# Kernel optimization log

Measured on AMD Instinct MI355X. Metric: run time of the kernel, lower is better.

Reference implementation:

```python
import jax, jax.numpy as jnp
import numpy as np


def setup_inputs() -> dict:
    key = jax.random.key(0)
    ks = jax.random.split(key, 4)
    B, S, D, U = 4, 4096, 128, 64
    x = jax.random.normal(ks[0], (B, S, D), dtype=jnp.float32)
    Wq = jax.random.normal(ks[1], (D, U), dtype=jnp.float32) * (1.0 / np.sqrt(D))
    Wk = jax.random.normal(ks[2], (D, U), dtype=jnp.float32) * (1.0 / np.sqrt(D))
    Wv = jax.random.normal(ks[3], (D, U), dtype=jnp.float32) * (1.0 / np.sqrt(D))
    bq = jnp.zeros((U,), dtype=jnp.float32)
    bk = jnp.zeros((U,), dtype=jnp.float32)
    bv = jnp.zeros((U,), dtype=jnp.float32)
    return {"x": x, "Wq": Wq, "bq": bq, "Wk": Wk, "bk": bk, "Wv": Wv, "bv": bv}


def reference(x, Wq, bq, Wk, bk, Wv, bv):
    # Single-head, unscaled, unmasked attention (faithful to the Keras layer).
    q = jnp.einsum("bsd,du->bsu", x, Wq) + bq  # [B,S,U]
    k = jnp.einsum("bsd,du->bsu", x, Wk) + bk  # [B,S,U]
    v = jnp.einsum("bsd,du->bsu", x, Wv) + bv  # [B,S,U]
    scores = jnp.einsum("bsu,btu->bst", q, k)  # [B,S,S], no 1/sqrt(d) scaling
    attn = jax.nn.softmax(scores, axis=-1)
    return jnp.einsum("bst,btu->bsu", attn, v)  # [B,S,U]
```

## Files before the change

### kernel.cpp

```cpp
#include <hip/hip_runtime.h>
#include <hip/hip_fp16.h>
#include <math.h>

#define SEQ   4096
#define DIM   128
#define UDIM  64
#define BATCH 4
#define BS    (BATCH*SEQ)

typedef _Float16 h8 __attribute__((ext_vector_type(8)));
typedef _Float16 h4 __attribute__((ext_vector_type(4)));
typedef _Float16 h2 __attribute__((ext_vector_type(2)));
typedef float    f4 __attribute__((ext_vector_type(4)));

#define MFMA_K32(a,b,c) __builtin_amdgcn_mfma_f32_16x16x32_f16((a),(b),(c),0,0,0)
#define MFMA_K16(a,b,c) __builtin_amdgcn_mfma_f32_16x16x16f16((a),(b),(c),0,0,0)

__device__ __forceinline__ h2 pk2(float a, float b) {
  return __builtin_bit_cast(h2, __builtin_amdgcn_cvt_pkrtz(a, b));
}
__device__ __forceinline__ float fexp2(float x) {
#if __has_builtin(__builtin_amdgcn_exp2f)
  return __builtin_amdgcn_exp2f(x);
#else
  return exp2f(x);
#endif
}

#define WT_STRIDE 272
#define KB_STRIDE 144
#define L2E 1.44269504088896f


__global__ __launch_bounds__(256, 3) void proj_mfma(
    const float* __restrict__ x,
    const float* __restrict__ Wq, const float* __restrict__ bq,
    const float* __restrict__ Wk, const float* __restrict__ bk,
    const float* __restrict__ Wv, const float* __restrict__ bv,
    _Float16* __restrict__ qf, _Float16* __restrict__ kswz, _Float16* __restrict__ vswz)
{
  const int proj = blockIdx.y;
  const float* __restrict__ W    = proj==0 ? Wq : (proj==1 ? Wk : Wv);
  const float* __restrict__ bias = proj==0 ? bq : (proj==1 ? bk : bv);
  const int tid  = threadIdx.x;
  const int lane = tid & 63, wv = tid >> 6;
  const int n = lane & 15, quad = lane >> 4;
  const int r0 = blockIdx.x * 64;

  __shared__ __align__(16) char lds[UDIM * WT_STRIDE];
  __shared__ __align__(16) char kbnc[4 * 16 * KB_STRIDE];

  #pragma unroll
  for (int i = 0; i < 8; ++i) {
    const int idx = i*256 + tid;
    const int nn  = idx & 63;
    const int k4  = (idx >> 6) * 4;
    const float w0 = W[(k4+0)*UDIM + nn];
    const float w1 = W[(k4+1)*UDIM + nn];
    const float w2 = W[(k4+2)*UDIM + nn];
    const float w3 = W[(k4+3)*UDIM + nn];
    int2 wd;
    wd.x = __builtin_bit_cast(int, pk2(w0, w1));
    wd.y = __builtin_bit_cast(int, pk2(w2, w3));
    *(int2*)(lds + nn*WT_STRIDE + k4*2) = wd;
  }
  __syncthreads();

  const int row = r0 + wv*16 + n;
  h8 xa[4];
  #pragma unroll
  for (int ks = 0; ks < 4; ++ks) {
    const float* xp = x + (size_t)row*DIM + ks*32 + quad*8;
    const f4 a = *(const f4*)xp, b = *(const f4*)(xp + 4);
    int4 pkd;
    pkd.x = __builtin_bit_cast(int, pk2(a[0], a[1]));
    pkd.y = __builtin_bit_cast(int, pk2(a[2], a[3]));
    pkd.z = __builtin_bit_cast(int, pk2(b[0], b[1]));
    pkd.w = __builtin_bit_cast(int, pk2(b[2], b[3]));
    xa[ks] = __builtin_bit_cast(h8, pkd);
  }

  f4 acc[4];
  #pragma unroll
  for (int nt = 0; nt < 4; ++nt) acc[nt] = (f4){0.f,0.f,0.f,0.f};

  #pragma unroll
  for (int ks = 0; ks < 4; ++ks)
    #pragma unroll
    for (int nt = 0; nt < 4; ++nt) {
      const h8 wf = *(const h8*)(lds + (nt*16 + n)*WT_STRIDE + (ks*32 + quad*8)*2);
      acc[nt] = MFMA_K32(xa[ks], wf, acc[nt]);
    }

  #pragma unroll
  for (int nt = 0; nt < 4; ++nt) {
    const float bb = bias[nt*16 + n];
    #pragma unroll
    for (int r = 0; r < 4; ++r) acc[nt][r] += bb;
  }

  const int b  = r0 / SEQ;
  const int kb = ((r0 % SEQ) >> 4) + wv;

  if (proj == 0) {
    #pragma unroll
    for (int nt = 0; nt < 4; ++nt)
      #pragma unroll
      for (int r = 0; r < 4; ++r) acc[nt][r] *= L2E;
    const int par = lane & 1;
    const unsigned sel = par ? 0x03020706u : 0x05040100u;
    #pragma unroll
    for (int nt = 0; nt < 4; ++nt)
      #pragma unroll
      for (int p = 0; p < 2; ++p) {
        const int r = 2*p;
        unsigned A  = __builtin_bit_cast(unsigned, pk2(acc[nt][r], acc[nt][r+1]));
        unsigned Bs = (unsigned)__builtin_amdgcn_mov_dpp((int)A, 0xB1, 0xF, 0xF, true);
        unsigned w  = __builtin_amdgcn_perm(Bs, A, sel);
        const int orow = r0 + wv*16 + 4*quad + r + par;
        const int ocol = nt*16 + n - par;
        *(unsigned*)((char*)qf + ((size_t)orow*UDIM + ocol)*2) = w;
      }
  } else if (proj == 1) {
    char* base = kbnc + wv*(16*KB_STRIDE);
    #pragma unroll
    for (int nt = 0; nt < 4; ++nt)
      #pragma unroll
      for (int r = 0; r < 4; ++r)
        *(_Float16*)(base + (4*quad + r)*KB_STRIDE + (nt*16 + n)*2) =
            (_Float16)acc[nt][r];
    _Float16* kdst = kswz + (size_t)b*SEQ*UDIM;
    #pragma unroll
    for (int ks = 0; ks < 2; ++ks) {
      const h8 f = *(const h8*)(base + n*KB_STRIDE + ks*64 + quad*16);
      *(h8*)(kdst + ((size_t)(kb*2 + ks)*64 + lane)*8) = f;
    }
  } else {
    _Float16* vdst = vswz + (size_t)b*SEQ*UDIM;
    #pragma unroll
    for (int pr = 0; pr < 2; ++pr) {
      int4 t;
      t.x = __builtin_bit_cast(int, pk2(acc[2*pr][0],   acc[2*pr][1]));
      t.y = __builtin_bit_cast(int, pk2(acc[2*pr][2],   acc[2*pr][3]));
      t.z = __builtin_bit_cast(int, pk2(acc[2*pr+1][0], acc[2*pr+1][1]));
      t.w = __builtin_bit_cast(int, pk2(acc[2*pr+1][2], acc[2*pr+1][3]));
      *(int4*)(vdst + ((size_t)(kb*2 + pr)*64 + lane)*8) = t;
    }
  }
}

__global__ __launch_bounds__(256, 4) void flash_attn_t(
    const _Float16* __restrict__ qf, const _Float16* __restrict__ kswz,
    const _Float16* __restrict__ vswz,
    _Float16* __restrict__ opart, float* __restrict__ Mp, float* __restrict__ Lp,
    int nkt)
{
  const int qt = blockIdx.x, b = blockIdx.y, sp = blockIdx.z;
  const int tid = threadIdx.x;
  const int lane = tid & 63, wid = tid >> 6;
  const int n = lane & 15, quad = lane >> 4;
  const int qbase = qt*128 + wid*32;

  const _Float16* __restrict__ qb = qf + (size_t)b*SEQ*UDIM;
  const _Float16* kpl = kswz + (size_t)b*SEQ*UDIM + (size_t)sp*nkt*4096 + lane*8;
  const _Float16* kph = kpl + 2048;
  const _Float16* vpl = vswz + (size_t)b*SEQ*UDIM + (size_t)sp*nkt*4096 + lane*8;
  const _Float16* vph = vpl + 2048;

  h8 qB[2][2];
  #pragma unroll
  for (int nt = 0; nt < 2; ++nt)
    #pragma unroll
    for (int ks = 0; ks < 2; ++ks)
      qB[nt][ks] = *(const h8*)(qb + (size_t)(qbase + nt*16 + n)*UDIM + ks*32 + quad*8);

  f4 O[4][2], Ol[2];
  #pragma unroll
  for (int ut = 0; ut < 4; ++ut)
    #pragma unroll
    for (int nt = 0; nt < 2; ++nt) O[ut][nt] = (f4){0.f,0.f,0.f,0.f};
  Ol[0] = (f4){0.f,0.f,0.f,0.f};
  Ol[1] = (f4){0.f,0.f,0.f,0.f};

  float M[2] = {-1e30f, -1e30f};

  h4 ones_a;
  { const _Float16 o = (_Float16)1.0f;
    ones_a[0]=o; ones_a[1]=o; ones_a[2]=o; ones_a[3]=o; }

  for (int t = 0; t < nkt; ++t) {
    h8 ka[4][2];
    ka[0][0] = *(const h8*)(kpl);        ka[0][1] = *(const h8*)(kpl +  512);
    ka[1][0] = *(const h8*)(kpl + 1024); ka[1][1] = *(const h8*)(kpl + 1536);
    ka[2][0] = *(const h8*)(kph);        ka[2][1] = *(const h8*)(kph +  512);
    ka[3][0] = *(const h8*)(kph + 1024); ka[3][1] = *(const h8*)(kph + 1536);

    h8 vc0 = *(const h8*)(vpl);
    h8 vc1 = *(const h8*)(vpl + 512);

    f4 S[4][2];
    #pragma unroll
    for (int mt = 0; mt < 4; ++mt)
      #pragma unroll
      for (int nt = 0; nt < 2; ++nt) S[mt][nt] = (f4){0.f,0.f,0.f,0.f};
    #pragma unroll
    for (int ks = 0; ks < 2; ++ks)
      #pragma unroll
      for (int mt = 0; mt < 4; ++mt)
        #pragma unroll
        for (int nt = 0; nt < 2; ++nt)
          S[mt][nt] = MFMA_K32(ka[mt][ks], qB[nt][ks], S[mt][nt]);

    float mn[2];
    #pragma unroll
    for (int nt = 0; nt < 2; ++nt) {
      float m0 = fmaxf(fmaxf(S[0][nt][0], S[0][nt][1]), fmaxf(S[0][nt][2], S[0][nt][3]));
      float m1 = fmaxf(fmaxf(S[1][nt][0], S[1][nt][1]), fmaxf(S[1][nt][2], S[1][nt][3]));
      float m2 = fmaxf(fmaxf(S[2][nt][0], S[2][nt][1]), fmaxf(S[2][nt][2], S[2][nt][3]));
      float m3 = fmaxf(fmaxf(S[3][nt][0], S[3][nt][1]), fmaxf(S[3][nt][2], S[3][nt][3]));
      float rm = fmaxf(fmaxf(m0, m1), fmaxf(m2, m3));
      rm = fmaxf(rm, __shfl_xor(rm, 16));
      rm = fmaxf(rm, __shfl_xor(rm, 32));
      mn[nt] = fmaxf(M[nt], rm);
    }

    const bool nochange = (mn[0] == M[0]) && (mn[1] == M[1]);
    if (!__all(nochange)) {
      #pragma unroll
      for (int nt = 0; nt < 2; ++nt) {
        const float alpha = fexp2(M[nt] - mn[nt]);
        #pragma unroll
        for (int ut = 0; ut < 4; ++ut)
          #pragma unroll
          for (int r = 0; r < 4; ++r) O[ut][nt][r] *= alpha;
        #pragma unroll
        for (int r = 0; r < 4; ++r) Ol[nt][r] *= alpha;
      }
    }
    M[0] = mn[0]; M[1] = mn[1];

    h4 pB[4][2];
    #pragma unroll
    for (int mt = 0; mt < 4; ++mt)
      #pragma unroll
      for (int nt = 0; nt < 2; ++nt) {
        #pragma unroll
        for (int r = 0; r < 4; ++r)
          S[mt][nt][r] = fexp2(S[mt][nt][r] - mn[nt]);
        int2 tt;
        tt.x = __builtin_bit_cast(int, pk2(S[mt][nt][0], S[mt][nt][1]));
        tt.y = __builtin_bit_cast(int, pk2(S[mt][nt][2], S[mt][nt][3]));
        pB[mt][nt] = __builtin_bit_cast(h4, tt);
      }

    #pragma unroll
    for (int mt = 0; mt < 4; ++mt) {
      h8 vn0, vn1;
      if (mt == 0) { vn0 = *(const h8*)(vpl + 1024); vn1 = *(const h8*)(vpl + 1536); }
      if (mt == 1) { vn0 = *(const h8*)(vph);        vn1 = *(const h8*)(vph +  512); }
      if (mt == 2) { vn0 = *(const h8*)(vph + 1024); vn1 = *(const h8*)(vph + 1536); }
      const int4 vi0 = __builtin_bit_cast(int4, vc0);
      const int4 vi1 = __builtin_bit_cast(int4, vc1);
      int2 p01, p23, p45, p67;
      p01.x = vi0.x; p01.y = vi0.y;  p23.x = vi0.z; p23.y = vi0.w;
      p45.x = vi1.x; p45.y = vi1.y;  p67.x = vi1.z; p67.y = vi1.w;
      h4 va[4];
      va[0] = __builtin_bit_cast(h4, p01);
      va[1] = __builtin_bit_cast(h4, p23);
      va[2] = __builtin_bit_cast(h4, p45);
      va[3] = __builtin_bit_cast(h4, p67);
      #pragma unroll
      for (int ut = 0; ut < 4; ++ut)
        #pragma unroll
        for (int nt = 0; nt < 2; ++nt)
          O[ut][nt] = MFMA_K16(va[ut], pB[mt][nt], O[ut][nt]);
      #pragma unroll
      for (int nt = 0; nt < 2; ++nt)
        Ol[nt] = MFMA_K16(ones_a, pB[mt][nt], Ol[nt]);
      if (mt < 3) { vc0 = vn0; vc1 = vn1; }
    }

    kpl += 4096; kph += 4096; vpl += 4096; vph += 4096;
  }

  const size_t rowg = (size_t)sp*BS + (size_t)b*SEQ + qbase;
  #pragma unroll
  for (int nt = 0; nt < 2; ++nt) {
    char* __restrict__ orow = (char*)(opart + (rowg + nt*16 + n)*UDIM);
    #pragma unroll
    for (int ut = 0; ut < 4; ++ut)
      #pragma unroll
      for (int p = 0; p < 2; ++p)
        *(unsigned*)(orow + (ut*16 + quad*4 + 2*p)*2) =
            __builtin_bit_cast(unsigned, pk2(O[ut][nt][2*p], O[ut][nt][2*p+1]));
    if (quad == 0) {
      Mp[rowg + nt*16 + n] = M[nt];
      Lp[rowg + nt*16 + n] = Ol[nt][0];
    }
  }
}

__global__ __launch_bounds__(256) void merge_out(
    const _Float16* __restrict__ opart, const float* __restrict__ Mp,
    const float* __restrict__ Lp, float* __restrict__ out, int nsplit)
{
  const int tid = threadIdx.x;
  const int row = blockIdx.x*16 + (tid >> 4);
  const int u4  = (tid & 15) * 4;
  float M = -1e30f;
  for (int s = 0; s < nsplit; ++s) M = fmaxf(M, Mp[(size_t)s*BS + row]);
  f4 num = (f4){0.f,0.f,0.f,0.f};
  float den = 0.f;
  for (int s = 0; s < nsplit; ++s) {
    const float w = fexp2(Mp[(size_t)s*BS + row] - M);
    den += w * Lp[(size_t)s*BS + row];
    const h4 op = *(const h4*)(opart + ((size_t)s*BS + row)*UDIM + u4);
    #pragma unroll
    for (int i = 0; i < 4; ++i) num[i] += w * (float)op[i];
  }
  const float dinv = 1.f / den;
  *(f4*)(out + (size_t)row*UDIM + u4) = num * dinv;
}

extern "C" void kernel_launch(void* const* d_in, const int* in_sizes, int n_in,
                              void* d_out, int out_size, void* d_ws, size_t ws_size,
                              hipStream_t stream) {
  (void)in_sizes; (void)n_in; (void)out_size;
  const float* x  = (const float*)d_in[0];
  const float* Wq = (const float*)d_in[1];
  const float* bq = (const float*)d_in[2];
  const float* Wk = (const float*)d_in[3];
  const float* bk = (const float*)d_in[4];
  const float* Wv = (const float*)d_in[5];
  const float* bv = (const float*)d_in[6];
  float* out = (float*)d_out;

  char* ws = (char*)d_ws;
  const size_t fBytes = (size_t)BS * UDIM * 2;
  auto need = [](int nsp) {
    return (size_t)3*BS*UDIM*2 + (size_t)nsp*BS*4*2 + (size_t)nsp*BS*UDIM*2;
  };
  int nsplit;
  if      (ws_size >= need(16)) nsplit = 16;
  else if (ws_size >= need(8))  nsplit = 8;
  else if (ws_size >= need(4))  nsplit = 4;
  else if (ws_size >= need(2))  nsplit = 2;
  else                          nsplit = 1;

  _Float16* qf   = (_Float16*)(ws);
  _Float16* kswz = (_Float16*)(ws + fBytes);
  _Float16* vswz = (_Float16*)(ws + 2*fBytes);
  float* Mp      = (float*)(ws + 3*fBytes);
  float* Lp      = (float*)(ws + 3*fBytes + (size_t)nsplit*BS*4);
  _Float16* opart = (_Float16*)(ws + 3*fBytes + (size_t)nsplit*BS*8);

  proj_mfma<<<dim3(BS/64, 3), 256, 0, stream>>>(x, Wq, bq, Wk, bk, Wv, bv, qf, kswz, vswz);
  flash_attn_t<<<dim3(SEQ/128, BATCH, nsplit), 256, 0, stream>>>(
      qf, kswz, vswz, opart, Mp, Lp, (SEQ/64)/nsplit);
  merge_out<<<dim3(BS/16), 256, 0, stream>>>(opart, Mp, Lp, out, nsplit);
}
```

Baseline: 123.0 us.

## Fuse QKV projections per block, prefetch K tiles, cap split-K at 8

The projection kernel now computes Q, K and V in one block from a single read of x, with all three weight matrices staged in shared memory, instead of launching one block per projection. This removes the repeated x reads and cuts the launch count. The attention loop now loads the next K tile right after the score MFMAs, so the load overlaps the softmax and PV work. The attention occupancy hint drops from 4 to 3 and the maximum split count drops from 16 to 8, which reduces merge traffic but may lower parallelism and raise register pressure.

```diff
diff --git a/kernel.cpp b/kernel.cpp
--- a/kernel.cpp
+++ b/kernel.cpp
@@ -32,39 +32,39 @@
 #define L2E 1.44269504088896f
 
 
-__global__ __launch_bounds__(256, 3) void proj_mfma(
+__global__ __launch_bounds__(256, 2) void proj_mfma(
     const float* __restrict__ x,
     const float* __restrict__ Wq, const float* __restrict__ bq,
     const float* __restrict__ Wk, const float* __restrict__ bk,
     const float* __restrict__ Wv, const float* __restrict__ bv,
     _Float16* __restrict__ qf, _Float16* __restrict__ kswz, _Float16* __restrict__ vswz)
 {
-  const int proj = blockIdx.y;
-  const float* __restrict__ W    = proj==0 ? Wq : (proj==1 ? Wk : Wv);
-  const float* __restrict__ bias = proj==0 ? bq : (proj==1 ? bk : bv);
   const int tid  = threadIdx.x;
   const int lane = tid & 63, wv = tid >> 6;
   const int n = lane & 15, quad = lane >> 4;
   const int r0 = blockIdx.x * 64;
 
-  __shared__ __align__(16) char lds[UDIM * WT_STRIDE];
+  __shared__ __align__(16) char wlds[3][UDIM * WT_STRIDE];
   __shared__ __align__(16) char kbnc[4 * 16 * KB_STRIDE];
 
   #pragma unroll
-  for (int i = 0; i < 8; ++i) {
-    const int idx = i*256 + tid;
-    const int nn  = idx & 63;
-    const int k4  = (idx >> 6) * 4;
-    const float w0 = W[(k4+0)*UDIM + nn];
-    const float w1 = W[(k4+1)*UDIM + nn];
-    const float w2 = W[(k4+2)*UDIM + nn];
-    const float w3 = W[(k4+3)*UDIM + nn];
-    int2 wd;
-    wd.x = __builtin_bit_cast(int, pk2(w0, w1));
-    wd.y = __builtin_bit_cast(int, pk2(w2, w3));
-    *(int2*)(lds + nn*WT_STRIDE + k4*2) = wd;
-  }
-  __syncthreads();
+  for (int p = 0; p < 3; ++p) {
+    const float* __restrict__ W = (p == 0) ? Wq : ((p == 1) ? Wk : Wv);
+    #pragma unroll
+    for (int i = 0; i < 8; ++i) {
+      const int idx = i*256 + tid;
+      const int nn  = idx & 63;
+      const int k4  = (idx >> 6) * 4;
+      const float w0 = W[(k4+0)*UDIM + nn];
+      const float w1 = W[(k4+1)*UDIM + nn];
+      const float w2 = W[(k4+2)*UDIM + nn];
+      const float w3 = W[(k4+3)*UDIM + nn];
+      int2 wd;
+      wd.x = __builtin_bit_cast(int, pk2(w0, w1));
+      wd.y = __builtin_bit_cast(int, pk2(w2, w3));
+      *(int2*)(wlds[p] + nn*WT_STRIDE + k4*2) = wd;
+    }
+  }
 
   const int row = r0 + wv*16 + n;
   h8 xa[4];
@@ -79,77 +79,80 @@
     pkd.w = __builtin_bit_cast(int, pk2(b[2], b[3]));
     xa[ks] = __builtin_bit_cast(h8, pkd);
   }
-
-  f4 acc[4];
-  #pragma unroll
-  for (int nt = 0; nt < 4; ++nt) acc[nt] = (f4){0.f,0.f,0.f,0.f};
-
-  #pragma unroll
-  for (int ks = 0; ks < 4; ++ks)
-    #pragma unroll
-    for (int nt = 0; nt < 4; ++nt) {
-      const h8 wf = *(const h8*)(lds + (nt*16 + n)*WT_STRIDE + (ks*32 + quad*8)*2);
-      acc[nt] = MFMA_K32(xa[ks], wf, acc[nt]);
-    }
-
-  #pragma unroll
-  for (int nt = 0; nt < 4; ++nt) {
-    const float bb = bias[nt*16 + n];
-    #pragma unroll
-    for (int r = 0; r < 4; ++r) acc[nt][r] += bb;
-  }
+  __syncthreads();
 
   const int b  = r0 / SEQ;
   const int kb = ((r0 % SEQ) >> 4) + wv;
 
-  if (proj == 0) {
-    #pragma unroll
-    for (int nt = 0; nt < 4; ++nt)
-      #pragma unroll
-      for (int r = 0; r < 4; ++r) acc[nt][r] *= L2E;
-    const int par = lane & 1;
-    const unsigned sel = par ? 0x03020706u : 0x05040100u;
-    #pragma unroll
-    for (int nt = 0; nt < 4; ++nt)
-      #pragma unroll
-      for (int p = 0; p < 2; ++p) {
-        const int r = 2*p;
-        unsigned A  = __builtin_bit_cast(unsigned, pk2(acc[nt][r], acc[nt][r+1]));
-        unsigned Bs = (unsigned)__builtin_amdgcn_mov_dpp((int)A, 0xB1, 0xF, 0xF, true);
-        unsigned w  = __builtin_amdgcn_perm(Bs, A, sel);
-        const int orow = r0 + wv*16 + 4*quad + r + par;
-        const int ocol = nt*16 + n - par;
-        *(unsigned*)((char*)qf + ((size_t)orow*UDIM + ocol)*2) = w;
-      }
-  } else if (proj == 1) {
-    char* base = kbnc + wv*(16*KB_STRIDE);
-    #pragma unroll
-    for (int nt = 0; nt < 4; ++nt)
-      #pragma unroll
-      for (int r = 0; r < 4; ++r)
-        *(_Float16*)(base + (4*quad + r)*KB_STRIDE + (nt*16 + n)*2) =
-            (_Float16)acc[nt][r];
-    _Float16* kdst = kswz + (size_t)b*SEQ*UDIM;
-    #pragma unroll
-    for (int ks = 0; ks < 2; ++ks) {
-      const h8 f = *(const h8*)(base + n*KB_STRIDE + ks*64 + quad*16);
-      *(h8*)(kdst + ((size_t)(kb*2 + ks)*64 + lane)*8) = f;
-    }
-  } else {
-    _Float16* vdst = vswz + (size_t)b*SEQ*UDIM;
-    #pragma unroll
-    for (int pr = 0; pr < 2; ++pr) {
-      int4 t;
-      t.x = __builtin_bit_cast(int, pk2(acc[2*pr][0],   acc[2*pr][1]));
-      t.y = __builtin_bit_cast(int, pk2(acc[2*pr][2],   acc[2*pr][3]));
-      t.z = __builtin_bit_cast(int, pk2(acc[2*pr+1][0], acc[2*pr+1][1]));
-      t.w = __builtin_bit_cast(int, pk2(acc[2*pr+1][2], acc[2*pr+1][3]));
-      *(int4*)(vdst + ((size_t)(kb*2 + pr)*64 + lane)*8) = t;
-    }
-  }
-}
-
-__global__ __launch_bounds__(256, 4) void flash_attn_t(
+  #pragma unroll
+  for (int p = 0; p < 3; ++p) {
+    const float* __restrict__ bias = (p == 0) ? bq : ((p == 1) ? bk : bv);
+    f4 acc[4];
+    #pragma unroll
+    for (int nt = 0; nt < 4; ++nt) acc[nt] = (f4){0.f,0.f,0.f,0.f};
+    #pragma unroll
+    for (int ks = 0; ks < 4; ++ks)
+      #pragma unroll
+      for (int nt = 0; nt < 4; ++nt) {
+        const h8 wf = *(const h8*)(wlds[p] + (nt*16 + n)*WT_STRIDE + (ks*32 + quad*8)*2);
+        acc[nt] = MFMA_K32(xa[ks], wf, acc[nt]);
+      }
+    #pragma unroll
+    for (int nt = 0; nt < 4; ++nt) {
+      const float bb = bias[nt*16 + n];
+      #pragma unroll
+      for (int r = 0; r < 4; ++r) acc[nt][r] += bb;
+    }
+
+    if (p == 0) {
+      #pragma unroll
+      for (int nt = 0; nt < 4; ++nt)
+        #pragma unroll
+        for (int r = 0; r < 4; ++r) acc[nt][r] *= L2E;
+      const int par = lane & 1;
+      const unsigned sel = par ? 0x03020706u : 0x05040100u;
+      #pragma unroll
+      for (int nt = 0; nt < 4; ++nt)
+        #pragma unroll
+        for (int pp = 0; pp < 2; ++pp) {
+          const int r = 2*pp;
+          unsigned A  = __builtin_bit_cast(unsigned, pk2(acc[nt][r], acc[nt][r+1]));
+          unsigned Bs = (unsigned)__builtin_amdgcn_mov_dpp((int)A, 0xB1, 0xF, 0xF, true);
+          unsigned w  = __builtin_amdgcn_perm(Bs, A, sel);
+          const int orow = r0 + wv*16 + 4*quad + r + par;
+          const int ocol = nt*16 + n - par;
+          *(unsigned*)((char*)qf + ((size_t)orow*UDIM + ocol)*2) = w;
+        }
+    } else if (p == 1) {
+      char* base = kbnc + wv*(16*KB_STRIDE);
+      #pragma unroll
+      for (int nt = 0; nt < 4; ++nt)
+        #pragma unroll
+        for (int r = 0; r < 4; ++r)
+          *(_Float16*)(base + (4*quad + r)*KB_STRIDE + (nt*16 + n)*2) =
+              (_Float16)acc[nt][r];
+      _Float16* kdst = kswz + (size_t)b*SEQ*UDIM;
+      #pragma unroll
+      for (int ks = 0; ks < 2; ++ks) {
+        const h8 f = *(const h8*)(base + n*KB_STRIDE + ks*64 + quad*16);
+        *(h8*)(kdst + ((size_t)(kb*2 + ks)*64 + lane)*8) = f;
+      }
+    } else {
+      _Float16* vdst = vswz + (size_t)b*SEQ*UDIM;
+      #pragma unroll
+      for (int pr = 0; pr < 2; ++pr) {
+        int4 t;
+        t.x = __builtin_bit_cast(int, pk2(acc[2*pr][0],   acc[2*pr][1]));
+        t.y = __builtin_bit_cast(int, pk2(acc[2*pr][2],   acc[2*pr][3]));
+        t.z = __builtin_bit_cast(int, pk2(acc[2*pr+1][0], acc[2*pr+1][1]));
+        t.w = __builtin_bit_cast(int, pk2(acc[2*pr+1][2], acc[2*pr+1][3]));
+        *(int4*)(vdst + ((size_t)(kb*2 + pr)*64 + lane)*8) = t;
+      }
+    }
+  }
+}
+
+__global__ __launch_bounds__(256, 3) void flash_attn_t(
     const _Float16* __restrict__ qf, const _Float16* __restrict__ kswz,
     const _Float16* __restrict__ vswz,
     _Float16* __restrict__ opart, float* __restrict__ Mp, float* __restrict__ Lp,
@@ -188,13 +191,13 @@
   { const _Float16 o = (_Float16)1.0f;
     ones_a[0]=o; ones_a[1]=o; ones_a[2]=o; ones_a[3]=o; }
 
+  h8 ka[4][2];
+  ka[0][0] = *(const h8*)(kpl);        ka[0][1] = *(const h8*)(kpl +  512);
+  ka[1][0] = *(const h8*)(kpl + 1024); ka[1][1] = *(const h8*)(kpl + 1536);
+  ka[2][0] = *(const h8*)(kph);        ka[2][1] = *(const h8*)(kph +  512);
+  ka[3][0] = *(const h8*)(kph + 1024); ka[3][1] = *(const h8*)(kph + 1536);
+
   for (int t = 0; t < nkt; ++t) {
-    h8 ka[4][2];
-    ka[0][0] = *(const h8*)(kpl);        ka[0][1] = *(const h8*)(kpl +  512);
-    ka[1][0] = *(const h8*)(kpl + 1024); ka[1][1] = *(const h8*)(kpl + 1536);
-    ka[2][0] = *(const h8*)(kph);        ka[2][1] = *(const h8*)(kph +  512);
-    ka[3][0] = *(const h8*)(kph + 1024); ka[3][1] = *(const h8*)(kph + 1536);
-
     h8 vc0 = *(const h8*)(vpl);
     h8 vc1 = *(const h8*)(vpl + 512);
 
@@ -210,6 +213,15 @@
         #pragma unroll
         for (int nt = 0; nt < 2; ++nt)
           S[mt][nt] = MFMA_K32(ka[mt][ks], qB[nt][ks], S[mt][nt]);
+
+    const bool more = (t + 1 < nkt);
+    if (more) {
+      kpl += 4096; kph += 4096;
+      ka[0][0] = *(const h8*)(kpl);        ka[0][1] = *(const h8*)(kpl +  512);
+      ka[1][0] = *(const h8*)(kpl + 1024); ka[1][1] = *(const h8*)(kpl + 1536);
+      ka[2][0] = *(const h8*)(kph);        ka[2][1] = *(const h8*)(kph +  512);
+      ka[3][0] = *(const h8*)(kph + 1024); ka[3][1] = *(const h8*)(kph + 1536);
+    }
 
     float mn[2];
     #pragma unroll
@@ -280,7 +292,7 @@
       if (mt < 3) { vc0 = vn0; vc1 = vn1; }
     }
 
-    kpl += 4096; kph += 4096; vpl += 4096; vph += 4096;
+    vpl += 4096; vph += 4096;
   }
 
   const size_t rowg = (size_t)sp*BS + (size_t)b*SEQ + qbase;
@@ -341,11 +353,10 @@
     return (size_t)3*BS*UDIM*2 + (size_t)nsp*BS*4*2 + (size_t)nsp*BS*UDIM*2;
   };
   int nsplit;
-  if      (ws_size >= need(16)) nsplit = 16;
-  else if (ws_size >= need(8))  nsplit = 8;
-  else if (ws_size >= need(4))  nsplit = 4;
-  else if (ws_size >= need(2))  nsplit = 2;
-  else                          nsplit = 1;
+  if      (ws_size >= need(8)) nsplit = 8;
+  else if (ws_size >= need(4)) nsplit = 4;
+  else if (ws_size >= need(2)) nsplit = 2;
+  else                         nsplit = 1;
 
   _Float16* qf   = (_Float16*)(ws);
   _Float16* kswz = (_Float16*)(ws + fBytes);
@@ -354,7 +365,7 @@
   float* Lp      = (float*)(ws + 3*fBytes + (size_t)nsplit*BS*4);
   _Float16* opart = (_Float16*)(ws + 3*fBytes + (size_t)nsplit*BS*8);
 
-  proj_mfma<<<dim3(BS/64, 3), 256, 0, stream>>>(x, Wq, bq, Wk, bk, Wv, bv, qf, kswz, vswz);
+  proj_mfma<<<dim3(BS/64), 256, 0, stream>>>(x, Wq, bq, Wk, bk, Wv, bv, qf, kswz, vswz);
   flash_attn_t<<<dim3(SEQ/128, BATCH, nsplit), 256, 0, stream>>>(
       qf, kswz, vswz, opart, Mp, Lp, (SEQ/64)/nsplit);
   merge_out<<<dim3(BS/16), 256, 0, stream>>>(opart, Mp, Lp, out, nsplit);
```

Result: faster. 111.7 us (-9.2%).
